# Kernel optimization log

Hardware: AMD Instinct MI355X
Metric: run time of the kernel (lower is better)

The kernel has to match this reference:

```python
import jax, jax.numpy as jnp
import numpy as np

TOP_K = 8
EPS = 1e-12  # matches torch F.normalize default eps

def _l2_normalize(x, axis=-1):
    norm = jnp.linalg.norm(x, axis=axis, keepdims=True)
    return x / jnp.maximum(norm, EPS)

def setup_inputs() -> dict:
    key = jax.random.key(0)
    k1, k2 = jax.random.split(key)
    hidden_states = jax.random.normal(k1, (16384, 2048), dtype=jnp.float32)
    proto = jax.random.normal(k2, (64, 2048), dtype=jnp.float32) * 0.02
    return {"hidden_states": hidden_states, "proto": proto}

def reference(hidden_states, proto):
    # L2-normalize tokens and expert prototypes, cosine-similarity logits
    h = _l2_normalize(hidden_states, axis=1)          # [T, D]
    p = _l2_normalize(proto, axis=1)                  # [E, D]
    router_logits = jnp.einsum('td,ed->te', h, p)     # [T, E]
    routing_weights = jax.nn.softmax(router_logits.astype(jnp.float32), axis=1)
    routing_weights, selected_experts = jax.lax.top_k(routing_weights, TOP_K)
    return routing_weights, selected_experts
```

## Files before the change

### kernel.cpp

```cpp
#include <hip/hip_runtime.h>
#include <math.h>

#define NTOK   16384
#define DIM    2048
#define NEXP   64
#define TOPK   8
#define TB     16
#define KC     64
#define NCHUNK (DIM / KC)
#define XLS    20
#define NLIMB  4

typedef int    v4i __attribute__((ext_vector_type(4)));
typedef double v4d __attribute__((ext_vector_type(4)));

#define WS_NEEDED (512 + (size_t)NEXP * NLIMB * (DIM / 4) * 4)

#define XSCALE 134217728.0f
#define PSCALE 8589934592.0f
#define BIAS   0x80808080u

__device__ __constant__ double CWD4[7] = {
    8.673617379884035e-19, 2.220446049250313e-16, 5.684341886080802e-14,
    1.4551915228366852e-11, 3.725290298461914e-09, 9.5367431640625e-07,
    2.44140625e-04};

__global__ __launch_bounds__(64) void proto_prep_kernel(
    const float* __restrict__ proto, double* __restrict__ pinv,
    int* __restrict__ plimb)
{
    const int e = blockIdx.x, t = threadIdx.x;
    const float* row = proto + (size_t)e * DIM;
    const int k0 = t * 32;
    double s = 0.0;
#pragma unroll
    for (int g = 0; g < 8; ++g) {
        unsigned pk0 = 0, pk1 = 0, pk2 = 0, pk3 = 0;
#pragma unroll
        for (int b = 0; b < 4; ++b) {
            float f = row[k0 + g * 4 + b];
            s += (double)f * (double)f;
            int u = (int)rintf(f * PSCALE);
            unsigned ub = (unsigned)u + BIAS;
            pk0 |= ( ub        & 255u) << (8 * b);
            pk1 |= ((ub >>  8) & 255u) << (8 * b);
            pk2 |= ((ub >> 16) & 255u) << (8 * b);
            pk3 |= ( ub >> 24        ) << (8 * b);
        }
        const int dw = (k0 + g * 4) >> 2;
        plimb[(e * NLIMB + 0) * (DIM / 4) + dw] = (int)(pk0 ^ BIAS);
        plimb[(e * NLIMB + 1) * (DIM / 4) + dw] = (int)(pk1 ^ BIAS);
        plimb[(e * NLIMB + 2) * (DIM / 4) + dw] = (int)(pk2 ^ BIAS);
        plimb[(e * NLIMB + 3) * (DIM / 4) + dw] = (int)(pk3 ^ BIAS);
    }
#pragma unroll
    for (int d = 1; d < 64; d <<= 1)
        s += __shfl_xor(s, d, 64);
    if (t == 0)
        pinv[e] = 1.0 / fmax(sqrt(s), 1e-12);
}

#define MF(A, B, C) __builtin_amdgcn_mfma_i32_16x16x64_i8(A, B, C, 0, 0, 0)

#define BURST16(AF, B0, B1, B2, B3) do {                                                \
    acc[0]=MF(AF[0],B0,acc[0]); acc[1]=MF(AF[1],B0,acc[1]);                             \
    acc[2]=MF(AF[2],B0,acc[2]); acc[3]=MF(AF[3],B0,acc[3]);                             \
    acc[1]=MF(AF[0],B1,acc[1]); acc[2]=MF(AF[1],B1,acc[2]);                             \
    acc[3]=MF(AF[2],B1,acc[3]); acc[4]=MF(AF[3],B1,acc[4]);                             \
    acc[2]=MF(AF[0],B2,acc[2]); acc[3]=MF(AF[1],B2,acc[3]);                             \
    acc[4]=MF(AF[2],B2,acc[4]); acc[5]=MF(AF[3],B2,acc[5]);                             \
    acc[3]=MF(AF[0],B3,acc[3]); acc[4]=MF(AF[1],B3,acc[4]);                             \
    acc[5]=MF(AF[2],B3,acc[5]); acc[6]=MF(AF[3],B3,acc[6]);                             \
} while (0)

#define LOADAF(cur) do {                                         \
    af[0] = *(const v4i*)&xl[cur][0][arow][akg * 4];             \
    af[1] = *(const v4i*)&xl[cur][1][arow][akg * 4];             \
    af[2] = *(const v4i*)&xl[cur][2][arow][akg * 4];             \
    af[3] = *(const v4i*)&xl[cur][3][arow][akg * 4];             \
} while (0)

#define LOADB(c) do {                                            \
    const int* _bp = bbase + (c) * 16;                           \
    bf0 = *(const v4i*)(_bp);                                    \
    bf1 = *(const v4i*)(_bp + 1 * (DIM / 4));                    \
    bf2 = *(const v4i*)(_bp + 2 * (DIM / 4));                    \
    bf3 = *(const v4i*)(_bp + 3 * (DIM / 4));                    \
} while (0)

__global__ __launch_bounds__(256, 2) void router_i8_kernel(
    const float* __restrict__ x, const double* __restrict__ pinv,
    const int* __restrict__ plimb, float* __restrict__ out)
{
    __shared__ __align__(16) int xl[2][NLIMB][TB][XLS];
    __shared__ float  logits[TB][NEXP];
    __shared__ double xinv_lds[TB];
    __shared__ double pinv_lds[NEXP];

    const int tid  = threadIdx.x;
    const int lane = tid & 63;
    const int w    = tid >> 6;
    const int tok0 = blockIdx.x * TB;

    const int td = tid >> 4;
    const int dw = tid & 15;
    const float* xsrc = x + (size_t)(tok0 + td) * DIM + dw * 4;

    const int arow = lane & 15;
    const int akg  = lane >> 4;
    const int ecol = w * 16 + arow;
    const int* bbase = plimb + (size_t)ecol * NLIMB * (DIM / 4) + akg * 4;

    v4i acc[7];
#pragma unroll
    for (int d = 0; d < 7; ++d) acc[d] = (v4i){0, 0, 0, 0};
    double sumsq = 0.0;

    if (tid < NEXP) pinv_lds[tid] = pinv[tid];

    auto decomp_store = [&](const float4 xq, int buf) {
        sumsq += (double)xq.x * xq.x + (double)xq.y * xq.y
               + (double)xq.z * xq.z + (double)xq.w * xq.w;
        unsigned b0 = (unsigned)(int)rintf(xq.x * XSCALE) + BIAS;
        unsigned b1 = (unsigned)(int)rintf(xq.y * XSCALE) + BIAS;
        unsigned b2 = (unsigned)(int)rintf(xq.z * XSCALE) + BIAS;
        unsigned b3 = (unsigned)(int)rintf(xq.w * XSCALE) + BIAS;
#pragma unroll
        for (int i = 0; i < NLIMB; ++i) {
            unsigned d = ((b0 >> (8 * i)) & 255u)
                       | (((b1 >> (8 * i)) & 255u) << 8)
                       | (((b2 >> (8 * i)) & 255u) << 16)
                       | (((b3 >> (8 * i)) & 255u) << 24);
            xl[buf][i][td][dw] = (int)(d ^ BIAS);
        }
    };

    v4i bf0, bf1, bf2, bf3;

    LOADB(0);
    float4 xv = *(const float4*)(xsrc);
    decomp_store(xv, 0);
    xv = *(const float4*)(xsrc + KC);
    asm volatile("s_waitcnt lgkmcnt(0)" ::: "memory");
    __builtin_amdgcn_sched_barrier(0);
    __builtin_amdgcn_s_barrier();

    for (int c = 0; c < NCHUNK; ++c) {
        const int cur = c & 1;

        v4i af[NLIMB];
        LOADAF(cur);
        if (c + 1 < NCHUNK) {
            decomp_store(xv, cur ^ 1);
            if (c + 2 < NCHUNK) xv = *(const float4*)(xsrc + (c + 2) * KC);
        }
        asm volatile("s_waitcnt lgkmcnt(0)" ::: "memory");
        __builtin_amdgcn_sched_barrier(0);

        __builtin_amdgcn_s_setprio(1);
        BURST16(af, bf0, bf1, bf2, bf3);
        __builtin_amdgcn_s_setprio(0);
        __builtin_amdgcn_sched_barrier(0);

        if (c + 1 < NCHUNK) LOADB(c + 1);
        __builtin_amdgcn_sched_barrier(0);
        __builtin_amdgcn_s_barrier();
    }

    sumsq += __shfl_xor(sumsq, 1, 16);
    sumsq += __shfl_xor(sumsq, 2, 16);
    sumsq += __shfl_xor(sumsq, 4, 16);
    sumsq += __shfl_xor(sumsq, 8, 16);
    if (dw == 0)
        xinv_lds[td] = 1.0 / fmax(sqrt(sumsq), 1e-12);

    const int ones = 0x01010101;
    v4i onesv = (v4i){ones, ones, ones, ones};
    int rp = arow * ones;
    v4i rowv = (v4i){rp, rp, rp, rp};
    v4i c1 = (v4i){0, 0, 0, 0}, c2 = (v4i){0, 0, 0, 0};
    c1 = __builtin_amdgcn_mfma_i32_16x16x64_i8(rowv, onesv, c1, 0, 0, 0);
    c2 = __builtin_amdgcn_mfma_i32_16x16x64_i8(onesv, rowv, c2, 0, 0, 0);
    __syncthreads();

#pragma unroll
    for (int i = 0; i < 4; ++i) {
        double S = 0.0;
#pragma unroll
        for (int d = 0; d < 7; ++d)
            S = fma((double)acc[d][i], CWD4[d], S);
        const int tr = c1[i] >> 6;
        const int ec = c2[i] >> 6;
        const int e  = w * 16 + ec;
        logits[tr][e] = (float)(S * xinv_lds[tr] * pinv_lds[e]);
    }
    __syncthreads();

#pragma unroll 1
    for (int i = 0; i < 4; ++i) {
        const int tl = w * 4 + i;
        const float l32 = logits[tl][lane];

        float m = l32;
#pragma unroll
        for (int d = 1; d < 64; d <<= 1) {
            float o = __shfl_xor(m, d, 64);
            m = fmaxf(m, o);
        }
        const float dd = l32 - m;
        const float e32 = (float)exp((double)dd);

        float r[8];
#pragma unroll
        for (int j = 0; j < 8; ++j) {
            float rj = __shfl(e32, j, 64);
#pragma unroll
            for (int b = 1; b < 8; ++b)
                rj += __shfl(e32, j + 8 * b, 64);
            r[j] = rj;
        }
        const float S = ((r[0] + r[1]) + (r[2] + r[3])) +
                        ((r[4] + r[5]) + (r[6] + r[7]));
        const float wgt = e32 / S;

        int rank = 0;
#pragma unroll 1
        for (int sdist = 1; sdist < 64; ++sdist) {
            float ow = __shfl_xor(wgt, sdist, 64);
            int j = lane ^ sdist;
            rank += (ow > wgt) || (ow == wgt && j < lane);
        }

        if (rank < TOPK) {
            const int tok = tok0 + tl;
            out[tok * TOPK + rank] = wgt;
            out[NTOK * TOPK + tok * TOPK + rank] = (float)lane;
        }
    }
}

__global__ __launch_bounds__(256, 2) void router_f64_kernel(
    const float* __restrict__ x, const float* __restrict__ proto,
    float* __restrict__ out)
{
    __shared__ float  logits[TB][NEXP];
    __shared__ double xinv_lds[TB];
    __shared__ double pinv_lds[NEXP];

    const int tid  = threadIdx.x;
    const int lane = tid & 63;
    const int w    = tid >> 6;
    const int tok0 = blockIdx.x * TB;
    const int etile = w;
    const int arow  = lane & 15;
    const int akg   = lane >> 4;
    const int kbase = akg * 8;

    v4d acc0 = {0., 0., 0., 0.}, acc1 = {0., 0., 0., 0.};
    v4d acc2 = {0., 0., 0., 0.}, acc3 = {0., 0., 0., 0.};
    double sumsq = 0.0, psq = 0.0;

    const float* xrow = x     + (size_t)(tok0 + arow)       * DIM + kbase;
    const float* prow = proto + (size_t)(etile * 16 + arow) * DIM + kbase;

    float4 xa0, xa1, pa0, pa1, xb0, xb1, pb0, pb1;

#define FLOADSET(X0, X1, P0, P1, c) do {                            \
    const float* _xp = xrow + (c) * 32;                             \
    const float* _pp = prow + (c) * 32;                             \
    X0 = *(const float4*)(_xp);  X1 = *(const float4*)(_xp + 4);    \
    P0 = *(const float4*)(_pp);  P1 = *(const float4*)(_pp + 4);    \
    } while (0)
#define FNORMQ(A, B) do {                                           \
    double a0 = (double)A.x, a1 = (double)A.y,                      \
           a2 = (double)A.z, a3 = (double)A.w;                      \
    double u0 = (double)B.x, u1 = (double)B.y,                      \
           u2 = (double)B.z, u3 = (double)B.w;                      \
    sumsq += a0*a0 + a1*a1 + a2*a2 + a3*a3;                         \
    psq   += u0*u0 + u1*u1 + u2*u2 + u3*u3;                         \
    } while (0)
#define FCOMPUTE(X0, X1, P0, P1) do {                               \
    FNORMQ(X0, P0); FNORMQ(X1, P1);                                 \
    acc0 = __builtin_amdgcn_mfma_f64_16x16x4f64((double)X0.x, (double)P0.x, acc0, 0, 0, 0); \
    acc1 = __builtin_amdgcn_mfma_f64_16x16x4f64((double)X0.y, (double)P0.y, acc1, 0, 0, 0); \
    acc2 = __builtin_amdgcn_mfma_f64_16x16x4f64((double)X0.z, (double)P0.z, acc2, 0, 0, 0); \
    acc3 = __builtin_amdgcn_mfma_f64_16x16x4f64((double)X0.w, (double)P0.w, acc3, 0, 0, 0); \
    acc0 = __builtin_amdgcn_mfma_f64_16x16x4f64((double)X1.x, (double)P1.x, acc0, 0, 0, 0); \
    acc1 = __builtin_amdgcn_mfma_f64_16x16x4f64((double)X1.y, (double)P1.y, acc1, 0, 0, 0); \
    acc2 = __builtin_amdgcn_mfma_f64_16x16x4f64((double)X1.z, (double)P1.z, acc2, 0, 0, 0); \
    acc3 = __builtin_amdgcn_mfma_f64_16x16x4f64((double)X1.w, (double)P1.w, acc3, 0, 0, 0); \
    } while (0)

    FLOADSET(xa0, xa1, pa0, pa1, 0);
    for (int c = 0; c < 64; c += 2) {
        FLOADSET(xb0, xb1, pb0, pb1, c + 1);
        FCOMPUTE(xa0, xa1, pa0, pa1);
        if (c + 2 < 64) FLOADSET(xa0, xa1, pa0, pa1, c + 2);
        FCOMPUTE(xb0, xb1, pb0, pb1);
    }
    const v4d acc = (acc0 + acc1) + (acc2 + acc3);

    sumsq += __shfl_xor(sumsq, 16, 64);
    sumsq += __shfl_xor(sumsq, 32, 64);
    psq   += __shfl_xor(psq, 16, 64);
    psq   += __shfl_xor(psq, 32, 64);
    if (akg == 0) {
        xinv_lds[arow]              = 1.0 / fmax(sqrt(sumsq), 1e-12);
        pinv_lds[etile * 16 + arow] = 1.0 / fmax(sqrt(psq), 1e-12);
    }
    v4d c1 = {0., 0., 0., 0.}, c2 = {0., 0., 0., 0.};
    c1 = __builtin_amdgcn_mfma_f64_16x16x4f64((double)arow, 1.0, c1, 0, 0, 0);
    c2 = __builtin_amdgcn_mfma_f64_16x16x4f64(1.0, (double)arow, c2, 0, 0, 0);
    __syncthreads();
#pragma unroll
    for (int i = 0; i < 4; ++i) {
        const int tr = (int)(c1[i] * 0.25);
        const int ec = (int)(c2[i] * 0.25);
        const int e  = etile * 16 + ec;
        logits[tr][e] = (float)(acc[i] * xinv_lds[tr] * pinv_lds[e]);
    }
    __syncthreads();
#pragma unroll 1
    for (int i = 0; i < 4; ++i) {
        const int tl = w * 4 + i;
        const float l32 = logits[tl][lane];
        float m = l32;
#pragma unroll
        for (int d = 1; d < 64; d <<= 1) {
            float o = __shfl_xor(m, d, 64);
            m = fmaxf(m, o);
        }
        const float dd = l32 - m;
        const float e32 = (float)exp((double)dd);
        float r[8];
#pragma unroll
        for (int j = 0; j < 8; ++j) {
            float rj = __shfl(e32, j, 64);
#pragma unroll
            for (int b = 1; b < 8; ++b)
                rj += __shfl(e32, j + 8 * b, 64);
            r[j] = rj;
        }
        const float S = ((r[0] + r[1]) + (r[2] + r[3])) +
                        ((r[4] + r[5]) + (r[6] + r[7]));
        const float wgt = e32 / S;
        int rank = 0;
#pragma unroll 1
        for (int sdist = 1; sdist < 64; ++sdist) {
            float ow = __shfl_xor(wgt, sdist, 64);
            int j = lane ^ sdist;
            rank += (ow > wgt) || (ow == wgt && j < lane);
        }
        if (rank < TOPK) {
            const int tok = tok0 + tl;
            out[tok * TOPK + rank] = wgt;
            out[NTOK * TOPK + tok * TOPK + rank] = (float)lane;
        }
    }
}

extern "C" void kernel_launch(void* const* d_in, const int* in_sizes, int n_in,
                              void* d_out, int out_size, void* d_ws, size_t ws_size,
                              hipStream_t stream) {
    const float* x     = (const float*)d_in[0];
    const float* proto = (const float*)d_in[1];
    float* out         = (float*)d_out;
    (void)in_sizes; (void)n_in; (void)out_size;

    if (ws_size >= WS_NEEDED) {
        double* pinv = (double*)d_ws;
        int*    plimb = (int*)((char*)d_ws + 512);
        proto_prep_kernel<<<NEXP, 64, 0, stream>>>(proto, pinv, plimb);
        router_i8_kernel<<<NTOK / TB, 256, 0, stream>>>(x, pinv, plimb, out);
    } else {
        router_f64_kernel<<<NTOK / TB, 256, 0, stream>>>(x, proto, out);
    }
}
```

Before: 100.4 us.

## Split K dimension across two wave groups in int8 router kernel

Doubles the block to 512 threads and splits the 2048-wide reduction into two halves, each handled by four waves with its own LDS double buffer. The partial int32 accumulators and the partial sums of squares are then combined through LDS before the logit, softmax and top-k stages. The aim is to halve the serial chunk loop per block and raise memory-level parallelism. The cost is extra LDS traffic, more barriers for the reduction, and half the waves sitting idle during the epilogue.

```diff
diff --git a/kernel.cpp b/kernel.cpp
--- a/kernel.cpp
+++ b/kernel.cpp
@@ -7,7 +7,8 @@
 #define TOPK   8
 #define TB     16
 #define KC     64
-#define NCHUNK (DIM / KC)
+#define KHALF  1024
+#define NPHASE (KHALF / KC)
 #define XLS    20
 #define NLIMB  4
 
@@ -73,14 +74,14 @@
     acc[5]=MF(AF[2],B3,acc[5]); acc[6]=MF(AF[3],B3,acc[6]);                             \
 } while (0)
 
-#define LOADAF(cur) do {                                         \
-    af[0] = *(const v4i*)&xl[cur][0][arow][akg * 4];             \
-    af[1] = *(const v4i*)&xl[cur][1][arow][akg * 4];             \
-    af[2] = *(const v4i*)&xl[cur][2][arow][akg * 4];             \
-    af[3] = *(const v4i*)&xl[cur][3][arow][akg * 4];             \
+#define LOADAF4(cur) do {                                        \
+    af[0] = *(const v4i*)&xl[cur][khalf][0][arow][akg * 4];      \
+    af[1] = *(const v4i*)&xl[cur][khalf][1][arow][akg * 4];      \
+    af[2] = *(const v4i*)&xl[cur][khalf][2][arow][akg * 4];      \
+    af[3] = *(const v4i*)&xl[cur][khalf][3][arow][akg * 4];      \
 } while (0)
 
-#define LOADB(c) do {                                            \
+#define LOADB4(c) do {                                           \
     const int* _bp = bbase + (c) * 16;                           \
     bf0 = *(const v4i*)(_bp);                                    \
     bf1 = *(const v4i*)(_bp + 1 * (DIM / 4));                    \
@@ -88,13 +89,14 @@
     bf3 = *(const v4i*)(_bp + 3 * (DIM / 4));                    \
 } while (0)
 
-__global__ __launch_bounds__(256, 2) void router_i8_kernel(
+__global__ __launch_bounds__(512, 6) void router_i8_kernel(
     const float* __restrict__ x, const double* __restrict__ pinv,
     const int* __restrict__ plimb, float* __restrict__ out)
 {
-    __shared__ __align__(16) int xl[2][NLIMB][TB][XLS];
+    __shared__ __align__(16) int xl[2][2][NLIMB][TB][XLS];
     __shared__ float  logits[TB][NEXP];
     __shared__ double xinv_lds[TB];
+    __shared__ double xpart[2][TB];
     __shared__ double pinv_lds[NEXP];
 
     const int tid  = threadIdx.x;
@@ -102,14 +104,18 @@
     const int w    = tid >> 6;
     const int tok0 = blockIdx.x * TB;
 
-    const int td = tid >> 4;
+    const int kp = tid >> 8;
+    const int td = (tid >> 4) & 15;
     const int dw = tid & 15;
-    const float* xsrc = x + (size_t)(tok0 + td) * DIM + dw * 4;
-
-    const int arow = lane & 15;
-    const int akg  = lane >> 4;
-    const int ecol = w * 16 + arow;
-    const int* bbase = plimb + (size_t)ecol * NLIMB * (DIM / 4) + akg * 4;
+    const float* xsrc = x + (size_t)(tok0 + td) * DIM + kp * KHALF + dw * 4;
+
+    const int etile = w & 3;
+    const int khalf = w >> 2;
+    const int arow  = lane & 15;
+    const int akg   = lane >> 4;
+    const int ecol  = etile * 16 + arow;
+    const int* bbase = plimb + (size_t)ecol * NLIMB * (DIM / 4)
+                             + khalf * (KHALF / 4) + akg * 4;
 
     v4i acc[7];
 #pragma unroll
@@ -131,13 +137,13 @@
                        | (((b1 >> (8 * i)) & 255u) << 8)
                        | (((b2 >> (8 * i)) & 255u) << 16)
                        | (((b3 >> (8 * i)) & 255u) << 24);
-            xl[buf][i][td][dw] = (int)(d ^ BIAS);
+            xl[buf][kp][i][td][dw] = (int)(d ^ BIAS);
         }
     };
 
     v4i bf0, bf1, bf2, bf3;
 
-    LOADB(0);
+    LOADB4(0);
     float4 xv = *(const float4*)(xsrc);
     decomp_store(xv, 0);
     xv = *(const float4*)(xsrc + KC);
@@ -145,14 +151,14 @@
     __builtin_amdgcn_sched_barrier(0);
     __builtin_amdgcn_s_barrier();
 
-    for (int c = 0; c < NCHUNK; ++c) {
+    for (int c = 0; c < NPHASE; ++c) {
         const int cur = c & 1;
 
         v4i af[NLIMB];
-        LOADAF(cur);
-        if (c + 1 < NCHUNK) {
+        LOADAF4(cur);
+        if (c + 1 < NPHASE) {
             decomp_store(xv, cur ^ 1);
-            if (c + 2 < NCHUNK) xv = *(const float4*)(xsrc + (c + 2) * KC);
+            if (c + 2 < NPHASE) xv = *(const float4*)(xsrc + (c + 2) * KC);
         }
         asm volatile("s_waitcnt lgkmcnt(0)" ::: "memory");
         __builtin_amdgcn_sched_barrier(0);
@@ -162,7 +168,7 @@
         __builtin_amdgcn_s_setprio(0);
         __builtin_amdgcn_sched_barrier(0);
 
-        if (c + 1 < NCHUNK) LOADB(c + 1);
+        if (c + 1 < NPHASE) LOADB4(c + 1);
         __builtin_amdgcn_sched_barrier(0);
         __builtin_amdgcn_s_barrier();
     }
@@ -172,7 +178,7 @@
     sumsq += __shfl_xor(sumsq, 4, 16);
     sumsq += __shfl_xor(sumsq, 8, 16);
     if (dw == 0)
-        xinv_lds[td] = 1.0 / fmax(sqrt(sumsq), 1e-12);
+        xpart[kp][td] = sumsq;
 
     const int ones = 0x01010101;
     v4i onesv = (v4i){ones, ones, ones, ones};
@@ -181,60 +187,99 @@
     v4i c1 = (v4i){0, 0, 0, 0}, c2 = (v4i){0, 0, 0, 0};
     c1 = __builtin_amdgcn_mfma_i32_16x16x64_i8(rowv, onesv, c1, 0, 0, 0);
     c2 = __builtin_amdgcn_mfma_i32_16x16x64_i8(onesv, rowv, c2, 0, 0, 0);
-    __syncthreads();
-
-#pragma unroll
-    for (int i = 0; i < 4; ++i) {
-        double S = 0.0;
-#pragma unroll
-        for (int d = 0; d < 7; ++d)
-            S = fma((double)acc[d][i], CWD4[d], S);
-        const int tr = c1[i] >> 6;
-        const int ec = c2[i] >> 6;
-        const int e  = w * 16 + ec;
-        logits[tr][e] = (float)(S * xinv_lds[tr] * pinv_lds[e]);
-    }
-    __syncthreads();
-
+
+    int* cb = (int*)xl;
+    if (w >= 4) {
+        int base = ((w - 4) * 64 + lane) * 16;
+#pragma unroll
+        for (int d = 0; d < 4; ++d) {
+            cb[base + 4 * d + 0] = acc[d][0]; cb[base + 4 * d + 1] = acc[d][1];
+            cb[base + 4 * d + 2] = acc[d][2]; cb[base + 4 * d + 3] = acc[d][3];
+        }
+    }
+    __syncthreads();
+    if (w < 4) {
+        int base = (w * 64 + lane) * 16;
+#pragma unroll
+        for (int d = 0; d < 4; ++d) {
+            acc[d][0] += cb[base + 4 * d + 0]; acc[d][1] += cb[base + 4 * d + 1];
+            acc[d][2] += cb[base + 4 * d + 2]; acc[d][3] += cb[base + 4 * d + 3];
+        }
+    }
+    if (tid < TB)
+        xinv_lds[tid] = 1.0 / fmax(sqrt(xpart[0][tid] + xpart[1][tid]), 1e-12);
+    __syncthreads();
+    if (w >= 4) {
+        int base = ((w - 4) * 64 + lane) * 12;
+#pragma unroll
+        for (int d = 0; d < 3; ++d) {
+            cb[base + 4 * d + 0] = acc[4 + d][0]; cb[base + 4 * d + 1] = acc[4 + d][1];
+            cb[base + 4 * d + 2] = acc[4 + d][2]; cb[base + 4 * d + 3] = acc[4 + d][3];
+        }
+    }
+    __syncthreads();
+    if (w < 4) {
+        int base = (w * 64 + lane) * 12;
+#pragma unroll
+        for (int d = 0; d < 3; ++d) {
+            acc[4 + d][0] += cb[base + 4 * d + 0]; acc[4 + d][1] += cb[base + 4 * d + 1];
+            acc[4 + d][2] += cb[base + 4 * d + 2]; acc[4 + d][3] += cb[base + 4 * d + 3];
+        }
+#pragma unroll
+        for (int i = 0; i < 4; ++i) {
+            double S = 0.0;
+#pragma unroll
+            for (int d = 0; d < 7; ++d)
+                S = fma((double)acc[d][i], CWD4[d], S);
+            const int tr = c1[i] >> 6;
+            const int ec = c2[i] >> 6;
+            const int e  = etile * 16 + ec;
+            logits[tr][e] = (float)(S * xinv_lds[tr] * pinv_lds[e]);
+        }
+    }
+    __syncthreads();
+
+    if (w < 4) {
 #pragma unroll 1
-    for (int i = 0; i < 4; ++i) {
-        const int tl = w * 4 + i;
-        const float l32 = logits[tl][lane];
-
-        float m = l32;
-#pragma unroll
-        for (int d = 1; d < 64; d <<= 1) {
-            float o = __shfl_xor(m, d, 64);
-            m = fmaxf(m, o);
-        }
-        const float dd = l32 - m;
-        const float e32 = (float)exp((double)dd);
-
-        float r[8];
-#pragma unroll
-        for (int j = 0; j < 8; ++j) {
-            float rj = __shfl(e32, j, 64);
-#pragma unroll
-            for (int b = 1; b < 8; ++b)
-                rj += __shfl(e32, j + 8 * b, 64);
-            r[j] = rj;
-        }
-        const float S = ((r[0] + r[1]) + (r[2] + r[3])) +
-                        ((r[4] + r[5]) + (r[6] + r[7]));
-        const float wgt = e32 / S;
-
-        int rank = 0;
+        for (int i = 0; i < 4; ++i) {
+            const int tl = w * 4 + i;
+            const float l32 = logits[tl][lane];
+
+            float m = l32;
+#pragma unroll
+            for (int d = 1; d < 64; d <<= 1) {
+                float o = __shfl_xor(m, d, 64);
+                m = fmaxf(m, o);
+            }
+            const float dd = l32 - m;
+            const float e32 = (float)exp((double)dd);
+
+            float r[8];
+#pragma unroll
+            for (int j = 0; j < 8; ++j) {
+                float rj = __shfl(e32, j, 64);
+#pragma unroll
+                for (int b = 1; b < 8; ++b)
+                    rj += __shfl(e32, j + 8 * b, 64);
+                r[j] = rj;
+            }
+            const float S = ((r[0] + r[1]) + (r[2] + r[3])) +
+                            ((r[4] + r[5]) + (r[6] + r[7]));
+            const float wgt = e32 / S;
+
+            int rank = 0;
 #pragma unroll 1
-        for (int sdist = 1; sdist < 64; ++sdist) {
-            float ow = __shfl_xor(wgt, sdist, 64);
-            int j = lane ^ sdist;
-            rank += (ow > wgt) || (ow == wgt && j < lane);
-        }
-
-        if (rank < TOPK) {
-            const int tok = tok0 + tl;
-            out[tok * TOPK + rank] = wgt;
-            out[NTOK * TOPK + tok * TOPK + rank] = (float)lane;
+            for (int sdist = 1; sdist < 64; ++sdist) {
+                float ow = __shfl_xor(wgt, sdist, 64);
+                int j = lane ^ sdist;
+                rank += (ow > wgt) || (ow == wgt && j < lane);
+            }
+
+            if (rank < TOPK) {
+                const int tok = tok0 + tl;
+                out[tok * TOPK + rank] = wgt;
+                out[NTOK * TOPK + tok * TOPK + rank] = (float)lane;
+            }
         }
     }
 }
@@ -371,7 +416,7 @@
         double* pinv = (double*)d_ws;
         int*    plimb = (int*)((char*)d_ws + 512);
         proto_prep_kernel<<<NEXP, 64, 0, stream>>>(proto, pinv, plimb);
-        router_i8_kernel<<<NTOK / TB, 256, 0, stream>>>(x, pinv, plimb, out);
+        router_i8_kernel<<<NTOK / TB, 512, 0, stream>>>(x, pinv, plimb, out);
     } else {
         router_f64_kernel<<<NTOK / TB, 256, 0, stream>>>(x, proto, out);
     }
```

Measured after the change: 109.4 us. 9.0% more time.

## Load token rows directly into MFMA registers, dropping LDS staging and barriers

Applied to the files above, without the earlier changes.

Each wave now reads its own 16-token x fragment straight from global memory and splits it into int8 limbs in registers. This removes the shared LDS buffer and the per-chunk block barriers. Loads are double-buffered in registers, two chunks per loop iteration. The cost is that all four waves load and decompose the same x data, roughly quadrupling the VALU limb and sum-of-squares work and the cache traffic. Register pressure also rises.

```diff
diff --git a/kernel.cpp b/kernel.cpp
--- a/kernel.cpp
+++ b/kernel.cpp
@@ -8,7 +8,6 @@
 #define TB     16
 #define KC     64
 #define NCHUNK (DIM / KC)
-#define XLS    20
 #define NLIMB  4
 
 typedef int    v4i __attribute__((ext_vector_type(4)));
@@ -73,26 +72,26 @@
     acc[5]=MF(AF[2],B3,acc[5]); acc[6]=MF(AF[3],B3,acc[6]);                             \
 } while (0)
 
-#define LOADAF(cur) do {                                         \
-    af[0] = *(const v4i*)&xl[cur][0][arow][akg * 4];             \
-    af[1] = *(const v4i*)&xl[cur][1][arow][akg * 4];             \
-    af[2] = *(const v4i*)&xl[cur][2][arow][akg * 4];             \
-    af[3] = *(const v4i*)&xl[cur][3][arow][akg * 4];             \
+#define LOADX(X0, X1, X2, X3, c) do {                            \
+    const float* _xp = xrow + (c) * KC;                          \
+    X0 = *(const float4*)(_xp);                                  \
+    X1 = *(const float4*)(_xp + 4);                              \
+    X2 = *(const float4*)(_xp + 8);                              \
+    X3 = *(const float4*)(_xp + 12);                             \
 } while (0)
 
-#define LOADB(c) do {                                            \
+#define LOADBR(B0, B1, B2, B3, c) do {                           \
     const int* _bp = bbase + (c) * 16;                           \
-    bf0 = *(const v4i*)(_bp);                                    \
-    bf1 = *(const v4i*)(_bp + 1 * (DIM / 4));                    \
-    bf2 = *(const v4i*)(_bp + 2 * (DIM / 4));                    \
-    bf3 = *(const v4i*)(_bp + 3 * (DIM / 4));                    \
+    B0 = *(const v4i*)(_bp);                                     \
+    B1 = *(const v4i*)(_bp + 1 * (DIM / 4));                     \
+    B2 = *(const v4i*)(_bp + 2 * (DIM / 4));                     \
+    B3 = *(const v4i*)(_bp + 3 * (DIM / 4));                     \
 } while (0)
 
 __global__ __launch_bounds__(256, 2) void router_i8_kernel(
     const float* __restrict__ x, const double* __restrict__ pinv,
     const int* __restrict__ plimb, float* __restrict__ out)
 {
-    __shared__ __align__(16) int xl[2][NLIMB][TB][XLS];
     __shared__ float  logits[TB][NEXP];
     __shared__ double xinv_lds[TB];
     __shared__ double pinv_lds[NEXP];
@@ -102,14 +101,13 @@
     const int w    = tid >> 6;
     const int tok0 = blockIdx.x * TB;
 
-    const int td = tid >> 4;
-    const int dw = tid & 15;
-    const float* xsrc = x + (size_t)(tok0 + td) * DIM + dw * 4;
-
-    const int arow = lane & 15;
-    const int akg  = lane >> 4;
-    const int ecol = w * 16 + arow;
-    const int* bbase = plimb + (size_t)ecol * NLIMB * (DIM / 4) + akg * 4;
+    const int etile = w;
+    const int arow  = lane & 15;
+    const int akg   = lane >> 4;
+
+    const float* xrow = x + (size_t)(tok0 + arow) * DIM + akg * 16;
+    const int* bbase = plimb + (size_t)(etile * 16 + arow) * NLIMB * (DIM / 4)
+                             + akg * 4;
 
     v4i acc[7];
 #pragma unroll
@@ -118,61 +116,69 @@
 
     if (tid < NEXP) pinv_lds[tid] = pinv[tid];
 
-    auto decomp_store = [&](const float4 xq, int buf) {
-        sumsq += (double)xq.x * xq.x + (double)xq.y * xq.y
-               + (double)xq.z * xq.z + (double)xq.w * xq.w;
-        unsigned b0 = (unsigned)(int)rintf(xq.x * XSCALE) + BIAS;
-        unsigned b1 = (unsigned)(int)rintf(xq.y * XSCALE) + BIAS;
-        unsigned b2 = (unsigned)(int)rintf(xq.z * XSCALE) + BIAS;
-        unsigned b3 = (unsigned)(int)rintf(xq.w * XSCALE) + BIAS;
+    auto COMPUTE = [&](const float4 q0, const float4 q1,
+                       const float4 q2, const float4 q3,
+                       const v4i B0, const v4i B1, const v4i B2, const v4i B3) {
+        sumsq += (double)q0.x * q0.x + (double)q0.y * q0.y
+               + (double)q0.z * q0.z + (double)q0.w * q0.w;
+        sumsq += (double)q1.x * q1.x + (double)q1.y * q1.y
+               + (double)q1.z * q1.z + (double)q1.w * q1.w;
+        sumsq += (double)q2.x * q2.x + (double)q2.y * q2.y
+               + (double)q2.z * q2.z + (double)q2.w * q2.w;
+        sumsq += (double)q3.x * q3.x + (double)q3.y * q3.y
+               + (double)q3.z * q3.z + (double)q3.w * q3.w;
+        unsigned u[4][4];
+        u[0][0] = (unsigned)(int)rintf(q0.x * XSCALE) + BIAS;
+        u[0][1] = (unsigned)(int)rintf(q0.y * XSCALE) + BIAS;
+        u[0][2] = (unsigned)(int)rintf(q0.z * XSCALE) + BIAS;
+        u[0][3] = (unsigned)(int)rintf(q0.w * XSCALE) + BIAS;
+        u[1][0] = (unsigned)(int)rintf(q1.x * XSCALE) + BIAS;
+        u[1][1] = (unsigned)(int)rintf(q1.y * XSCALE) + BIAS;
+        u[1][2] = (unsigned)(int)rintf(q1.z * XSCALE) + BIAS;
+        u[1][3] = (unsigned)(int)rintf(q1.w * XSCALE) + BIAS;
+        u[2][0] = (unsigned)(int)rintf(q2.x * XSCALE) + BIAS;
+        u[2][1] = (unsigned)(int)rintf(q2.y * XSCALE) + BIAS;
+        u[2][2] = (unsigned)(int)rintf(q2.z * XSCALE) + BIAS;
+        u[2][3] = (unsigned)(int)rintf(q2.w * XSCALE) + BIAS;
+        u[3][0] = (unsigned)(int)rintf(q3.x * XSCALE) + BIAS;
+        u[3][1] = (unsigned)(int)rintf(q3.y * XSCALE) + BIAS;
+        u[3][2] = (unsigned)(int)rintf(q3.z * XSCALE) + BIAS;
+        u[3][3] = (unsigned)(int)rintf(q3.w * XSCALE) + BIAS;
+        v4i af[NLIMB];
 #pragma unroll
         for (int i = 0; i < NLIMB; ++i) {
-            unsigned d = ((b0 >> (8 * i)) & 255u)
-                       | (((b1 >> (8 * i)) & 255u) << 8)
-                       | (((b2 >> (8 * i)) & 255u) << 16)
-                       | (((b3 >> (8 * i)) & 255u) << 24);
-            xl[buf][i][td][dw] = (int)(d ^ BIAS);
-        }
+#pragma unroll
+            for (int g = 0; g < 4; ++g) {
+                unsigned d = ((u[g][0] >> (8 * i)) & 255u)
+                           | (((u[g][1] >> (8 * i)) & 255u) << 8)
+                           | (((u[g][2] >> (8 * i)) & 255u) << 16)
+                           | (((u[g][3] >> (8 * i)) & 255u) << 24);
+                af[i][g] = (int)(d ^ BIAS);
+            }
+        }
+        BURST16(af, B0, B1, B2, B3);
     };
 
-    v4i bf0, bf1, bf2, bf3;
-
-    LOADB(0);
-    float4 xv = *(const float4*)(xsrc);
-    decomp_store(xv, 0);
-    xv = *(const float4*)(xsrc + KC);
-    asm volatile("s_waitcnt lgkmcnt(0)" ::: "memory");
-    __builtin_amdgcn_sched_barrier(0);
-    __builtin_amdgcn_s_barrier();
-
-    for (int c = 0; c < NCHUNK; ++c) {
-        const int cur = c & 1;
-
-        v4i af[NLIMB];
-        LOADAF(cur);
-        if (c + 1 < NCHUNK) {
-            decomp_store(xv, cur ^ 1);
-            if (c + 2 < NCHUNK) xv = *(const float4*)(xsrc + (c + 2) * KC);
-        }
-        asm volatile("s_waitcnt lgkmcnt(0)" ::: "memory");
-        __builtin_amdgcn_sched_barrier(0);
-
-        __builtin_amdgcn_s_setprio(1);
-        BURST16(af, bf0, bf1, bf2, bf3);
-        __builtin_amdgcn_s_setprio(0);
-        __builtin_amdgcn_sched_barrier(0);
-
-        if (c + 1 < NCHUNK) LOADB(c + 1);
-        __builtin_amdgcn_sched_barrier(0);
-        __builtin_amdgcn_s_barrier();
-    }
-
-    sumsq += __shfl_xor(sumsq, 1, 16);
-    sumsq += __shfl_xor(sumsq, 2, 16);
-    sumsq += __shfl_xor(sumsq, 4, 16);
-    sumsq += __shfl_xor(sumsq, 8, 16);
-    if (dw == 0)
-        xinv_lds[td] = 1.0 / fmax(sqrt(sumsq), 1e-12);
+    float4 xa0, xa1, xa2, xa3, xb0, xb1, xb2, xb3;
+    v4i    ba0, ba1, ba2, ba3, bb0, bb1, bb2, bb3;
+
+    LOADX(xa0, xa1, xa2, xa3, 0);
+    LOADBR(ba0, ba1, ba2, ba3, 0);
+    for (int c = 0; c < NCHUNK; c += 2) {
+        LOADX(xb0, xb1, xb2, xb3, c + 1);
+        LOADBR(bb0, bb1, bb2, bb3, c + 1);
+        COMPUTE(xa0, xa1, xa2, xa3, ba0, ba1, ba2, ba3);
+        if (c + 2 < NCHUNK) {
+            LOADX(xa0, xa1, xa2, xa3, c + 2);
+            LOADBR(ba0, ba1, ba2, ba3, c + 2);
+        }
+        COMPUTE(xb0, xb1, xb2, xb3, bb0, bb1, bb2, bb3);
+    }
+
+    sumsq += __shfl_xor(sumsq, 16, 64);
+    sumsq += __shfl_xor(sumsq, 32, 64);
+    if (akg == 0)
+        xinv_lds[arow] = 1.0 / fmax(sqrt(sumsq), 1e-12);
 
     const int ones = 0x01010101;
     v4i onesv = (v4i){ones, ones, ones, ones};
@@ -191,7 +197,7 @@
             S = fma((double)acc[d][i], CWD4[d], S);
         const int tr = c1[i] >> 6;
         const int ec = c2[i] >> 6;
-        const int e  = w * 16 + ec;
+        const int e  = etile * 16 + ec;
         logits[tr][e] = (float)(S * xinv_lds[tr] * pinv_lds[e]);
     }
     __syncthreads();
```

Result: slower. 149.0 us (+48.4%).
